# Kernel optimization log

Hardware: AMD Instinct MI355X
Metric: run time of the kernel (lower is better)

Reference implementation:

```python
import jax, jax.numpy as jnp
import numpy as np

D_MODEL = 2048
N_HEADS = 16
N_KV = 4
HEAD_DIM = D_MODEL // N_HEADS  # 128
KV_DIM = N_KV * HEAD_DIM       # 512
CLIP = 8.0
EPS = 1e-5
THETA = 500000.0


def setup_inputs() -> dict:
    key = jax.random.key(0)
    ks = jax.random.split(key, 12)
    B, T = 2, 2048
    std = 0.02
    return {
        "x": jax.random.normal(ks[0], (B, T, D_MODEL), jnp.float32),
        "wq": jax.random.normal(ks[1], (D_MODEL, D_MODEL), jnp.float32) * std,
        "bq": jnp.zeros((D_MODEL,), jnp.float32),
        "wk": jax.random.normal(ks[2], (KV_DIM, D_MODEL), jnp.float32) * std,
        "bk": jnp.zeros((KV_DIM,), jnp.float32),
        "wv": jax.random.normal(ks[3], (KV_DIM, D_MODEL), jnp.float32) * std,
        "bv": jnp.zeros((KV_DIM,), jnp.float32),
        "wo": jax.random.normal(ks[4], (D_MODEL, D_MODEL), jnp.float32) * std,
        "bo": jnp.zeros((D_MODEL,), jnp.float32),
        "q_gamma": jnp.ones((D_MODEL,), jnp.float32),
        "q_beta": jnp.zeros((D_MODEL,), jnp.float32),
        "k_gamma": jnp.ones((KV_DIM,), jnp.float32),
        "k_beta": jnp.zeros((KV_DIM,), jnp.float32),
    }


def _layernorm(x, gamma, beta):
    mu = jnp.mean(x, axis=-1, keepdims=True)
    var = jnp.mean(jnp.square(x - mu), axis=-1, keepdims=True)
    return (x - mu) * jax.lax.rsqrt(var + EPS) * gamma + beta


def _rope(q, k):
    # q: (B,T,H,Dh), k: (B,T,Hkv,Dh); non-interleaved rotate-half RoPE
    T = q.shape[1]
    half = HEAD_DIM // 2
    inv_freq = 1.0 / (THETA ** (jnp.arange(0, half, dtype=jnp.float32) * 2.0 / HEAD_DIM))
    freqs = jnp.arange(T, dtype=jnp.float32)[:, None] * inv_freq[None, :]  # (T, half)
    emb = jnp.concatenate([freqs, freqs], axis=-1)  # (T, Dh)
    cos = jnp.cos(emb)[None, :, None, :]
    sin = jnp.sin(emb)[None, :, None, :]

    def rot_half(x):
        x1, x2 = x[..., :half], x[..., half:]
        return jnp.concatenate([-x2, x1], axis=-1)

    q = q * cos + rot_half(q) * sin
    k = k * cos + rot_half(k) * sin
    return q, k


def reference(x, wq, bq, wk, bk, wv, bv, wo, bo, q_gamma, q_beta, k_gamma, k_beta):
    B, T, _ = x.shape
    q = x @ wq.T + bq            # (B,T,D)
    k = x @ wk.T + bk            # (B,T,KV_DIM)
    v = x @ wv.T + bv
    q = jnp.clip(q, -CLIP, CLIP)
    k = jnp.clip(k, -CLIP, CLIP)
    v = jnp.clip(v, -CLIP, CLIP)
    q = _layernorm(q, q_gamma, q_beta)
    k = _layernorm(k, k_gamma, k_beta)
    q = q.reshape(B, T, N_HEADS, HEAD_DIM)
    k = k.reshape(B, T, N_KV, HEAD_DIM)
    v = v.reshape(B, T, N_KV, HEAD_DIM)
    q, k = _rope(q, k)
    # to (B,H,T,Dh)
    q = q.transpose(0, 2, 1, 3)
    k = k.transpose(0, 2, 1, 3)
    v = v.transpose(0, 2, 1, 3)
    g = N_HEADS // N_KV
    # GQA repeat_interleave via broadcast: (B,Hkv,T,Dh) -> (B,H,T,Dh)
    k = jnp.broadcast_to(k[:, :, None], (B, N_KV, g, T, HEAD_DIM)).reshape(B, N_HEADS, T, HEAD_DIM)
    v = jnp.broadcast_to(v[:, :, None], (B, N_KV, g, T, HEAD_DIM)).reshape(B, N_HEADS, T, HEAD_DIM)
    scale = 1.0 / jnp.sqrt(jnp.float32(HEAD_DIM))
    scores = jnp.einsum('bhqd,bhkd->bhqk', q, k) * scale
    causal = jnp.tril(jnp.ones((T, T), dtype=bool))
    scores = jnp.where(causal[None, None], scores, jnp.finfo(scores.dtype).min)
    att = jax.nn.softmax(scores, axis=-1)
    out = jnp.einsum('bhqk,bhkd->bhqd', att, v)     # (B,H,T,Dh)
    out = out.transpose(0, 2, 1, 3).reshape(B, T, D_MODEL)
    return out @ wo.T + bo
```

## Files before the change

kernel.cpp:

```cpp
#include <hip/hip_runtime.h>
#include <hip/hip_bf16.h>
#include <math.h>

typedef __bf16 bf16;
typedef __attribute__((ext_vector_type(8))) bf16 bf16x8;
typedef __attribute__((ext_vector_type(2))) bf16 bf16x2;
typedef __attribute__((ext_vector_type(4))) float f32x4;

#define LOG2E 1.4426950408889634f
#define LOG2_THETA 18.931568569324174f

#if __has_builtin(__builtin_amdgcn_exp2f)
#define EXP2F __builtin_amdgcn_exp2f
#else
#define EXP2F exp2f
#endif

__device__ inline void async_cp16(const void* gptr, void* lptr) {
  __builtin_amdgcn_global_load_lds(
      (const __attribute__((address_space(1))) unsigned int*)gptr,
      (__attribute__((address_space(3))) unsigned int*)lptr, 16, 0, 0);
}

__global__ __launch_bounds__(256) void cast_all(
    const float* __restrict__ x,  const float* __restrict__ wq,
    const float* __restrict__ wk, const float* __restrict__ wv,
    const float* __restrict__ wo, bf16* __restrict__ xb,
    bf16* __restrict__ wqkvb, bf16* __restrict__ wob) {
  const int bx = blockIdx.x;
  const size_t gi = ((size_t)bx * 256 + threadIdx.x) * 8;
  const float* src;
  bf16* dst;
  if (bx < 4096)      { src = x  + gi;              dst = xb + gi; }
  else if (bx < 6144) { src = wq + (gi -  8388608); dst = wqkvb + (gi - 8388608); }
  else if (bx < 6656) { src = wk + (gi - 12582912); dst = wqkvb + 4194304 + (gi - 12582912); }
  else if (bx < 7168) { src = wv + (gi - 13631488); dst = wqkvb + 5242880 + (gi - 13631488); }
  else                { src = wo + (gi - 14680064); dst = wob + (gi - 14680064); }
  float4 a = *(const float4*)(src);
  float4 b = *(const float4*)(src + 4);
  bf16x8 o;
  o[0] = (bf16)a.x; o[1] = (bf16)a.y; o[2] = (bf16)a.z; o[3] = (bf16)a.w;
  o[4] = (bf16)b.x; o[5] = (bf16)b.y; o[6] = (bf16)b.z; o[7] = (bf16)b.w;
  *(bf16x8*)dst = o;
}

template <typename OUT_T, bool QKV, bool CLIP>
__global__ __launch_bounds__(256) void gemm_bt(
    const bf16* __restrict__ A, const bf16* __restrict__ W,
    const float* __restrict__ b0, const float* __restrict__ b1,
    const float* __restrict__ b2, OUT_T* __restrict__ C,
    int M, int N, int K) {
  __shared__ bf16 As[128 * 64];
  __shared__ bf16 Bs[128 * 64];
  const int m0 = blockIdx.x * 128, n0 = blockIdx.y * 128;
  const int t = threadIdx.x;
  const int w = t >> 6, lane = t & 63, quad = lane >> 4, l15 = lane & 15;
  const int sw = l15 & 7;
  const int wm = (w >> 1) * 64, wn = (w & 1) * 64;

  f32x4 acc[4][4];
#pragma unroll
  for (int i = 0; i < 4; i++)
#pragma unroll
    for (int j = 0; j < 4; j++) acc[i][j] = (f32x4)0.0f;

  int soff[4];
#pragma unroll
  for (int i = 0; i < 4; i++) {
    const int c = w * 256 + i * 64 + lane;
    const int r = c >> 3;
    const int sl = (c & 7) ^ (r & 7);
    soff[i] = r * K + sl * 8;
  }
  const bf16* Abase = A + (size_t)m0 * K;
  const bf16* Wbase = W + (size_t)n0 * K;

  for (int k0 = 0; k0 < K; k0 += 64) {
#pragma unroll
    for (int i = 0; i < 4; i++) {
      const int dst = (w * 256 + i * 64) * 16;
      async_cp16(Abase + k0 + soff[i], (char*)As + dst);
      async_cp16(Wbase + k0 + soff[i], (char*)Bs + dst);
    }
    __syncthreads();

#pragma unroll
    for (int kk = 0; kk < 2; kk++) {
      bf16x8 af[4], bfr[4];
#pragma unroll
      for (int i = 0; i < 4; i++)
        af[i] = *(const bf16x8*)(As + (wm + i * 16 + l15) * 64 +
                                 (((kk * 4 + quad) ^ sw) * 8));
#pragma unroll
      for (int j = 0; j < 4; j++)
        bfr[j] = *(const bf16x8*)(Bs + (wn + j * 16 + l15) * 64 +
                                  (((kk * 4 + quad) ^ sw) * 8));
#pragma unroll
      for (int i = 0; i < 4; i++)
#pragma unroll
        for (int j = 0; j < 4; j++)
          acc[i][j] = __builtin_amdgcn_mfma_f32_16x16x32_bf16(af[i], bfr[j], acc[i][j], 0, 0, 0);
    }
    __syncthreads();
  }

#pragma unroll
  for (int i = 0; i < 4; i++)
#pragma unroll
    for (int j = 0; j < 4; j++) {
      const int col = n0 + wn + j * 16 + l15;
      float bval;
      if (QKV) {
        if (col < 2048) bval = b0[col];
        else if (col < 2560) bval = b1[col - 2048];
        else bval = b2[col - 2560];
      } else {
        bval = b0[col];
      }
#pragma unroll
      for (int r = 0; r < 4; r++) {
        const int row = m0 + wm + i * 16 + quad * 4 + r;
        float v = acc[i][j][r] + bval;
        if (CLIP) v = fminf(fmaxf(v, -8.0f), 8.0f);
        C[(size_t)row * N + col] = (OUT_T)v;
      }
    }
}

__global__ __launch_bounds__(256) void fused_mid(
    const bf16* __restrict__ X, const float* __restrict__ qg,
    const float* __restrict__ qb, const float* __restrict__ kg,
    const float* __restrict__ kb, bf16* __restrict__ Qr,
    bf16* __restrict__ Kr, bf16* __restrict__ Vt) {
  __shared__ float smf[2056];
  __shared__ bf16 smt[64][136];
  const int bx = blockIdx.x;
  const int tid = threadIdx.x;
  const int w = tid >> 6, lane = tid & 63;
  float* red = smf + 2048;

  if (bx < 4096) {
    const int row = bx, b = row >> 11, tpos = row & 2047;
    const bf16* x = X + (size_t)row * 3072;
    bf16x8 xi = *(const bf16x8*)(x + tid * 8);
    float v[8];
    float s = 0.0f;
#pragma unroll
    for (int e = 0; e < 8; e++) { v[e] = (float)xi[e]; s += v[e]; }
#pragma unroll
    for (int m = 32; m >= 1; m >>= 1) s += __shfl_xor(s, m, 64);
    if (lane == 0) red[w] = s;
    __syncthreads();
    const float mean = (red[0] + red[1] + red[2] + red[3]) * (1.0f / 2048.0f);
    float vs = 0.0f;
#pragma unroll
    for (int e = 0; e < 8; e++) { float d = v[e] - mean; vs += d * d; }
#pragma unroll
    for (int m = 32; m >= 1; m >>= 1) vs += __shfl_xor(vs, m, 64);
    if (lane == 0) red[4 + w] = vs;
    __syncthreads();
    const float var = (red[4] + red[5] + red[6] + red[7]) * (1.0f / 2048.0f);
    const float rstd = rsqrtf(var + 1e-5f);
#pragma unroll
    for (int e = 0; e < 8; e++) {
      const int c = tid * 8 + e;
      const float y = (v[e] - mean) * rstd * qg[c] + qb[c];
      smf[c] = y; v[e] = y;
    }
    __syncthreads();
    const int c0 = tid * 8;
    const int h = c0 >> 7;
    bf16x8 ov;
#pragma unroll
    for (int e = 0; e < 8; e++) {
      const int c = c0 + e, d = c & 127, i = d & 63;
      const float inv = exp2f((float)i * (-LOG2_THETA / 64.0f));
      float sn, cs;
      sincosf((float)tpos * inv, &sn, &cs);
      const float rot = (d < 64) ? -smf[c + 64] : smf[c - 64];
      ov[e] = (bf16)(v[e] * cs + rot * sn);
    }
    *(bf16x8*)(Qr + ((size_t)(b * 16 + h) * 2048 + tpos) * 128 + (c0 & 127)) = ov;
  } else if (bx < 8192) {
    const int row = bx - 4096, b = row >> 11, tpos = row & 2047;
    const bf16* x = X + (size_t)row * 3072 + 2048;
    bf16x2 xi = *(const bf16x2*)(x + tid * 2);
    float v0 = (float)xi[0], v1 = (float)xi[1];
    float s = v0 + v1;
#pragma unroll
    for (int m = 32; m >= 1; m >>= 1) s += __shfl_xor(s, m, 64);
    if (lane == 0) red[w] = s;
    __syncthreads();
    const float mean = (red[0] + red[1] + red[2] + red[3]) * (1.0f / 512.0f);
    float d0 = v0 - mean, d1 = v1 - mean;
    float vs = d0 * d0 + d1 * d1;
#pragma unroll
    for (int m = 32; m >= 1; m >>= 1) vs += __shfl_xor(vs, m, 64);
    if (lane == 0) red[4 + w] = vs;
    __syncthreads();
    const float var = (red[4] + red[5] + red[6] + red[7]) * (1.0f / 512.0f);
    const float rstd = rsqrtf(var + 1e-5f);
    const int c0 = tid * 2;
    float y0 = d0 * rstd * kg[c0] + kb[c0];
    float y1 = d1 * rstd * kg[c0 + 1] + kb[c0 + 1];
    smf[c0] = y0; smf[c0 + 1] = y1;
    __syncthreads();
    const int kv = c0 >> 7;
    float yy[2] = {y0, y1};
    bf16x2 ov;
#pragma unroll
    for (int e = 0; e < 2; e++) {
      const int c = c0 + e, d = c & 127, i = d & 63;
      const float inv = exp2f((float)i * (-LOG2_THETA / 64.0f));
      float sn, cs;
      sincosf((float)tpos * inv, &sn, &cs);
      const float rot = (d < 64) ? -smf[c + 64] : smf[c - 64];
      ov[e] = (bf16)(yy[e] * cs + rot * sn);
    }
    *(bf16x2*)(Kr + ((size_t)(b * 4 + kv) * 2048 + tpos) * 128 + (c0 & 127)) = ov;
  } else {
    const int idx = bx - 8192;
    const int b = idx >> 7, kv = (idx >> 5) & 3, t0 = (idx & 31) * 64;
#pragma unroll
    for (int i = 0; i < 4; i++) {
      const int c = i * 256 + tid;
      const int r = c >> 4, d8 = (c & 15) * 8;
      *(bf16x8*)&smt[r][d8] =
          *(const bf16x8*)(X + (size_t)(b * 2048 + t0 + r) * 3072 + 2560 + kv * 128 + d8);
    }
    __syncthreads();
#pragma unroll
    for (int i = 0; i < 4; i++) {
      const int c = i * 256 + tid;
      const int d = c >> 3, t8 = (c & 7) * 8;
      bf16x8 o;
#pragma unroll
      for (int j = 0; j < 8; j++) o[j] = smt[t8 + j][d];
      *(bf16x8*)(Vt + (size_t)((b * 4 + kv) * 128 + d) * 2048 + t0 + t8) = o;
    }
  }
}

__global__ __launch_bounds__(256) void flash_attn(
    const bf16* __restrict__ Q, const bf16* __restrict__ Kt,
    const bf16* __restrict__ Vt, bf16* __restrict__ O) {
  const int p = blockIdx.x;
  const int h = blockIdx.y, b = blockIdx.z;
  const int kv = h >> 2;
  const int tid = threadIdx.x;
  const int w = tid >> 6, lane = tid & 63, quad = lane >> 4, l15 = lane & 15;

  __shared__ bf16 Ks[64][128];
  __shared__ bf16 Vs[128][64];
  __shared__ bf16 Ps[4][16][88];

  const bf16* Kb = Kt + (size_t)(b * 4 + kv) * 2048 * 128;
  const bf16* Vb = Vt + (size_t)(b * 4 + kv) * 128 * 2048;

  const int ksl = lane & 15, krt = lane >> 4;
  const int vsl = lane & 7,  vdt = lane >> 3;
  int okff[4], ovff[4];
#pragma unroll
  for (int i = 0; i < 4; i++) {
    const int c = w * 4 + i;
    const int rt = c * 4 + krt;
    okff[i] = rt * 128 + ((ksl ^ (rt & 15)) * 8);
    const int d = c * 8 + vdt;
    ovff[i] = d * 2048 + ((vsl ^ (d & 7)) * 8);
  }

  const float cexp = 0.08838834764831845f * LOG2E;
  bf16x8 ones;
#pragma unroll
  for (int i = 0; i < 8; i++) ones[i] = (bf16)1.0f;

#pragma unroll 1
  for (int pass = 0; pass < 2; pass++) {
    const int qb = (pass == 0) ? (31 - p) : p;
    const int q0 = qb * 64;
    const int nkt = qb + 1;

    const bf16* Qb = Q + ((size_t)(b * 16 + h) * 2048 + q0 + w * 16 + l15) * 128;
    bf16x8 aq[4];
#pragma unroll
    for (int kk = 0; kk < 4; kk++) aq[kk] = *(const bf16x8*)(Qb + kk * 32 + quad * 8);

    f32x4 o[9];
#pragma unroll
    for (int dt = 0; dt < 9; dt++) o[dt] = (f32x4)0.0f;

#pragma unroll 1
    for (int kt = 0; kt < nkt; kt++) {
      const int k0 = kt * 64;
      __syncthreads();
      {
        const size_t kbase = (size_t)k0 * 128;
#pragma unroll
        for (int i = 0; i < 4; i++) {
          const int c = w * 4 + i;
          async_cp16(Kb + kbase + okff[i], (char*)&Ks[0][0] + c * 1024);
          async_cp16(Vb + (size_t)k0 + ovff[i], (char*)&Vs[0][0] + c * 1024);
        }
      }
      __syncthreads();

      f32x4 s4[4];
#pragma unroll
      for (int j = 0; j < 4; j++) {
        f32x4 acc = (f32x4)0.0f;
        const int n = j * 16 + l15;
#pragma unroll
        for (int kk = 0; kk < 4; kk++) {
          bf16x8 bk = *(const bf16x8*)(
              &Ks[0][0] + n * 128 + (((kk * 4 + quad) ^ l15) * 8));
          acc = __builtin_amdgcn_mfma_f32_16x16x32_bf16(aq[kk], bk, acc, 0, 0, 0);
        }
        s4[j] = acc;
      }

      const bool diag = (kt == qb);
      const int qrow_base = q0 + w * 16 + quad * 4;
#pragma unroll
      for (int j = 0; j < 4; j++) {
        const int kg = k0 + j * 16 + l15;
#pragma unroll
        for (int r = 0; r < 4; r++) {
          float pv = EXP2F(s4[j][r] * cexp);
          if (diag && kg > qrow_base + r) pv = 0.0f;
          Ps[w][quad * 4 + r][j * 16 + l15] = (bf16)pv;
        }
      }
      __asm__ volatile("s_waitcnt lgkmcnt(0)" ::: "memory");

#pragma unroll
      for (int kk = 0; kk < 2; kk++) {
        bf16x8 pa = *(const bf16x8*)&Ps[w][l15][kk * 32 + quad * 8];
#pragma unroll
        for (int dt = 0; dt < 8; dt++) {
          const int d = dt * 16 + l15;
          bf16x8 vb = *(const bf16x8*)(
              &Vs[0][0] + d * 64 + (((kk * 4 + quad) ^ (d & 7)) * 8));
          o[dt] = __builtin_amdgcn_mfma_f32_16x16x32_bf16(pa, vb, o[dt], 0, 0, 0);
        }
        o[8] = __builtin_amdgcn_mfma_f32_16x16x32_bf16(pa, ones, o[8], 0, 0, 0);
      }
    }

    bf16* Ob = O + ((size_t)(b * 2048 + q0 + w * 16 + quad * 4)) * 2048 + h * 128;
#pragma unroll
    for (int r = 0; r < 4; r++) {
      const float rinv = 1.0f / o[8][r];
#pragma unroll
      for (int dt = 0; dt < 8; dt++)
        Ob[(size_t)r * 2048 + dt * 16 + l15] = (bf16)(o[dt][r] * rinv);
    }
  }
}

extern "C" void kernel_launch(void* const* d_in, const int* in_sizes, int n_in,
                              void* d_out, int out_size, void* d_ws, size_t ws_size,
                              hipStream_t stream) {
  const float* x   = (const float*)d_in[0];
  const float* wq  = (const float*)d_in[1];
  const float* bq  = (const float*)d_in[2];
  const float* wk  = (const float*)d_in[3];
  const float* bk  = (const float*)d_in[4];
  const float* wv  = (const float*)d_in[5];
  const float* bv  = (const float*)d_in[6];
  const float* wo  = (const float*)d_in[7];
  const float* bo  = (const float*)d_in[8];
  const float* qg  = (const float*)d_in[9];
  const float* qbt = (const float*)d_in[10];
  const float* kg  = (const float*)d_in[11];
  const float* kbt = (const float*)d_in[12];
  float* out = (float*)d_out;

  char* ws = (char*)d_ws;
  if (ws_size < (size_t)88080384) return;
  bf16* xb    = (bf16*)(ws);
  bf16* wqkvb = (bf16*)(ws + 16777216);
  bf16* wob   = (bf16*)(ws + 29360128);
  bf16* qkvb  = (bf16*)(ws + 37748736);
  bf16* Qr    = (bf16*)(ws + 62914560);
  bf16* Kr    = (bf16*)(ws + 79691776);
  bf16* Vt    = (bf16*)(ws + 83886080);
  bf16* At    = (bf16*)(ws);

  cast_all<<<9216, 256, 0, stream>>>(x, wq, wk, wv, wo, xb, wqkvb, wob);
  gemm_bt<bf16, true, true><<<dim3(32, 24), 256, 0, stream>>>(
      xb, wqkvb, bq, bk, bv, qkvb, 4096, 3072, 2048);
  fused_mid<<<8448, 256, 0, stream>>>(qkvb, qg, qbt, kg, kbt, Qr, Kr, Vt);
  flash_attn<<<dim3(16, 16, 2), 256, 0, stream>>>(Qr, Kr, Vt, At);
  gemm_bt<float, false, false><<<dim3(32, 16), 256, 0, stream>>>(
      At, wob, bo, nullptr, nullptr, out, 4096, 2048, 2048);
}
```

Measured before the change: 314.7 us.

## Double-buffer K/V tiles in flash attention with async prefetch

Adds two LDS buffers for K and V and issues the async global-to-LDS copy of the next key tile before computing the current one. A vmcnt wait replaces the full sync, so the load overlaps with the QK and PV MFMA work. It also raises wave priority around the MFMA sections. LDS use doubles, which may reduce occupancy. The loop's correctness now depends on the exact vmcnt count and the end-of-iteration barrier.

```diff
diff --git a/kernel.cpp b/kernel.cpp
--- a/kernel.cpp
+++ b/kernel.cpp
@@ -250,8 +250,8 @@
   const int tid = threadIdx.x;
   const int w = tid >> 6, lane = tid & 63, quad = lane >> 4, l15 = lane & 15;
 
-  __shared__ bf16 Ks[64][128];
-  __shared__ bf16 Vs[128][64];
+  __shared__ bf16 Ks[2][64][128];
+  __shared__ bf16 Vs[2][128][64];
   __shared__ bf16 Ps[4][16][88];
 
   const bf16* Kb = Kt + (size_t)(b * 4 + kv) * 2048 * 128;
@@ -269,6 +269,15 @@
     ovff[i] = d * 2048 + ((vsl ^ (d & 7)) * 8);
   }
 
+  auto stage = [&](int bufi, int k0) {
+#pragma unroll
+    for (int i = 0; i < 4; i++) {
+      const int c = w * 4 + i;
+      async_cp16(Kb + (size_t)k0 * 128 + okff[i], (char*)&Ks[bufi][0][0] + c * 1024);
+      async_cp16(Vb + (size_t)k0 + ovff[i], (char*)&Vs[bufi][0][0] + c * 1024);
+    }
+  };
+
   const float cexp = 0.08838834764831845f * LOG2E;
   bf16x8 ones;
 #pragma unroll
@@ -289,22 +298,23 @@
 #pragma unroll
     for (int dt = 0; dt < 9; dt++) o[dt] = (f32x4)0.0f;
 
+    stage(0, 0);
+
 #pragma unroll 1
     for (int kt = 0; kt < nkt; kt++) {
+      const int cur = kt & 1;
       const int k0 = kt * 64;
-      __syncthreads();
-      {
-        const size_t kbase = (size_t)k0 * 128;
-#pragma unroll
-        for (int i = 0; i < 4; i++) {
-          const int c = w * 4 + i;
-          async_cp16(Kb + kbase + okff[i], (char*)&Ks[0][0] + c * 1024);
-          async_cp16(Vb + (size_t)k0 + ovff[i], (char*)&Vs[0][0] + c * 1024);
-        }
-      }
-      __syncthreads();
+      if (kt + 1 < nkt) {
+        stage(cur ^ 1, k0 + 64);
+        __asm__ volatile("s_waitcnt vmcnt(8)" ::: "memory");
+      } else {
+        __asm__ volatile("s_waitcnt vmcnt(0)" ::: "memory");
+      }
+      __builtin_amdgcn_s_barrier();
+      __builtin_amdgcn_sched_barrier(0);
 
       f32x4 s4[4];
+      __builtin_amdgcn_s_setprio(1);
 #pragma unroll
       for (int j = 0; j < 4; j++) {
         f32x4 acc = (f32x4)0.0f;
@@ -312,11 +322,12 @@
 #pragma unroll
         for (int kk = 0; kk < 4; kk++) {
           bf16x8 bk = *(const bf16x8*)(
-              &Ks[0][0] + n * 128 + (((kk * 4 + quad) ^ l15) * 8));
+              &Ks[cur][0][0] + n * 128 + (((kk * 4 + quad) ^ l15) * 8));
           acc = __builtin_amdgcn_mfma_f32_16x16x32_bf16(aq[kk], bk, acc, 0, 0, 0);
         }
         s4[j] = acc;
       }
+      __builtin_amdgcn_s_setprio(0);
 
       const bool diag = (kt == qb);
       const int qrow_base = q0 + w * 16 + quad * 4;
@@ -332,6 +343,7 @@
       }
       __asm__ volatile("s_waitcnt lgkmcnt(0)" ::: "memory");
 
+      __builtin_amdgcn_s_setprio(1);
 #pragma unroll
       for (int kk = 0; kk < 2; kk++) {
         bf16x8 pa = *(const bf16x8*)&Ps[w][l15][kk * 32 + quad * 8];
@@ -339,11 +351,15 @@
         for (int dt = 0; dt < 8; dt++) {
           const int d = dt * 16 + l15;
           bf16x8 vb = *(const bf16x8*)(
-              &Vs[0][0] + d * 64 + (((kk * 4 + quad) ^ (d & 7)) * 8));
+              &Vs[cur][0][0] + d * 64 + (((kk * 4 + quad) ^ (d & 7)) * 8));
           o[dt] = __builtin_amdgcn_mfma_f32_16x16x32_bf16(pa, vb, o[dt], 0, 0, 0);
         }
         o[8] = __builtin_amdgcn_mfma_f32_16x16x32_bf16(pa, ones, o[8], 0, 0, 0);
       }
+      __builtin_amdgcn_s_setprio(0);
+
+      __builtin_amdgcn_sched_barrier(0);
+      __builtin_amdgcn_s_barrier();
     }
 
     bf16* Ob = O + ((size_t)(b * 2048 + q0 + w * 16 + quad * 4)) * 2048 + h * 128;
```

New measurement: 309.1 us. No clear change (-1.8%).
